# Kernel tuning notes

Measured on AMD Instinct MI355X. Metric: run time of the kernel, lower is better.

Reference implementation:

```python
import jax, jax.numpy as jnp
import numpy as np

D_MODEL = 1024
D_STATE = 16
N_LAYERS = 2
EXPAND = 2
D_CONV = 4
D_INNER = EXPAND * D_MODEL
DT_RANK = D_MODEL // 16  # 64
B, L = 2, 1024


def setup_inputs() -> dict:
    key = jax.random.key(0)
    ks = jax.random.split(key, 8)
    rn = lambda k, shape, s: jax.random.normal(k, shape, jnp.float32) * s
    x = rn(ks[0], (B, L, D_MODEL), 1.0)
    in_proj_w = rn(ks[1], (N_LAYERS, 2 * D_INNER, D_MODEL), D_MODEL ** -0.5)
    conv_w = rn(ks[2], (N_LAYERS, D_INNER, 1, D_CONV), D_CONV ** -0.5)
    conv_b = jnp.zeros((N_LAYERS, D_INNER), jnp.float32)
    x_proj_w = rn(ks[3], (N_LAYERS, DT_RANK + 2 * D_STATE, D_INNER), D_INNER ** -0.5)
    dt_proj_w = rn(ks[4], (N_LAYERS, D_INNER, DT_RANK), DT_RANK ** -0.5)
    dt_proj_b = rn(ks[5], (N_LAYERS, D_INNER), 0.1)
    # canonical Mamba init: A = -exp(A_log), A_log = log(1..d_state)
    A_log = jnp.tile(jnp.log(jnp.arange(1, D_STATE + 1, dtype=jnp.float32)), (N_LAYERS, D_INNER, 1))
    Dp = jnp.ones((N_LAYERS, D_INNER), jnp.float32)
    out_proj_w = rn(ks[6], (N_LAYERS, D_MODEL, D_INNER), D_INNER ** -0.5)
    ln_g = jnp.ones((N_LAYERS, D_MODEL), jnp.float32)
    ln_b = jnp.zeros((N_LAYERS, D_MODEL), jnp.float32)
    fn_g = jnp.ones((D_MODEL,), jnp.float32)
    fn_b = jnp.zeros((D_MODEL,), jnp.float32)
    return dict(x=x, ln_g=ln_g, ln_b=ln_b, in_proj_w=in_proj_w, conv_w=conv_w,
                conv_b=conv_b, x_proj_w=x_proj_w, dt_proj_w=dt_proj_w,
                dt_proj_b=dt_proj_b, A_log=A_log, Dp=Dp, out_proj_w=out_proj_w,
                fn_g=fn_g, fn_b=fn_b)


def _ln(x, g, b):
    m = jnp.mean(x, -1, keepdims=True)
    v = jnp.mean((x - m) ** 2, -1, keepdims=True)
    return (x - m) * jax.lax.rsqrt(v + 1e-5) * g + b


def _mamba_block(x, in_w, cw, cb, xpw, dtw, dtb, A_log, Dp, ow):
    Bb = x.shape[0]
    # input projection -> [B, L, 2*d_inner]
    xz = jnp.einsum('bld,ed->ble', x, in_w)
    u, res = jnp.split(xz, 2, axis=-1)
    # causal depthwise conv over time (torch: padding=3 then [..., :L])
    uc = jax.lax.conv_general_dilated(
        u.transpose(0, 2, 1), cw, (1,), [(D_CONV - 1, 0)],
        dimension_numbers=('NCH', 'OIH', 'NCH'), feature_group_count=D_INNER)
    u = jax.nn.silu(uc.transpose(0, 2, 1) + cb)  # [B, L, d_inner]
    # input-dependent dt, B, C
    xdbl = jnp.einsum('ble,fe->blf', u, xpw)
    dt, Bc, Cc = jnp.split(xdbl, [DT_RANK, DT_RANK + D_STATE], axis=-1)
    delta = jax.nn.softplus(jnp.einsum('blr,dr->bld', dt, dtw) + dtb)  # [B,L,d_inner]
    A = -jnp.exp(A_log)  # [d_inner, d_state]

    def step(h, inp):
        d_t, B_t, C_t, u_t = inp  # [B,d_inner],[B,d_state],[B,d_state],[B,d_inner]
        h = jnp.exp(d_t[:, :, None] * A) * h + (d_t * u_t)[:, :, None] * B_t[:, None, :]
        y = jnp.einsum('bds,bs->bd', h, C_t)
        return h, y

    xs = (delta.transpose(1, 0, 2), Bc.transpose(1, 0, 2),
          Cc.transpose(1, 0, 2), u.transpose(1, 0, 2))
    h0 = jnp.zeros((Bb, D_INNER, D_STATE), x.dtype)
    _, ys = jax.lax.scan(step, h0, xs)
    y = ys.transpose(1, 0, 2) + u * Dp
    y = y * jax.nn.silu(res)
    return jnp.einsum('ble,de->bld', y, ow)


def reference(x, ln_g, ln_b, in_proj_w, conv_w, conv_b, x_proj_w, dt_proj_w,
              dt_proj_b, A_log, Dp, out_proj_w, fn_g, fn_b):
    for i in range(N_LAYERS):
        x = x + _mamba_block(_ln(x, ln_g[i], ln_b[i]), in_proj_w[i], conv_w[i],
                             conv_b[i], x_proj_w[i], dt_proj_w[i], dt_proj_b[i],
                             A_log[i], Dp[i], out_proj_w[i])
    # dropout is identity in eval mode
    return _ln(x, fn_g, fn_b)
```

## Files before the change

kernel.cpp:

```cpp
#include <hip/hip_runtime.h>
#include <hip/hip_bf16.h>
#include <math.h>
#include <stdint.h>

#define DMODEL 1024
#define DSTATE 16
#define DINNER 2048
#define DTRANK 64
#define NB 2
#define LSEQ 1024
#define ROWS (NB*LSEQ)
#define NCH 64
#define LCH (LSEQ/NCH)
#define KSPLIT 8

typedef __bf16 bf16_t;
typedef __bf16 bf16x8 __attribute__((ext_vector_type(8)));
typedef __bf16 bf16x4 __attribute__((ext_vector_type(4)));
typedef float  f32x4  __attribute__((ext_vector_type(4)));

#define AS1(p) ((const __attribute__((address_space(1))) void*)(p))
#define AS3(p) ((__attribute__((address_space(3))) void*)(uint32_t)(uintptr_t)(p))

static __device__ __forceinline__ float sigmoidf_(float x){ return 1.f/(1.f+__expf(-x)); }
static __device__ __forceinline__ float softplusf_(float x){ return fmaxf(x,0.f) + log1pf(__expf(-fabsf(x))); }

__global__ __launch_bounds__(256) void cvt_kernel(const float* __restrict__ in,
    bf16_t* __restrict__ out, int n4)
{
  int i = blockIdx.x*256 + threadIdx.x;
  if (i < n4){
    float4 v = ((const float4*)in)[i];
    bf16x4 o = { (bf16_t)v.x, (bf16_t)v.y, (bf16_t)v.z, (bf16_t)v.w };
    ((bf16x4*)out)[i] = o;
  }
}

template<int OUTBF>
__global__ __launch_bounds__(256) void ln_kernel(const float* __restrict__ x,
    const float* __restrict__ g, const float* __restrict__ b,
    float* __restrict__ outf, bf16_t* __restrict__ outb)
{
  int row = blockIdx.x;
  float4 v = ((const float4*)(x + (size_t)row*DMODEL))[threadIdx.x];
  float s  = v.x+v.y+v.z+v.w;
  float s2 = v.x*v.x+v.y*v.y+v.z*v.z+v.w*v.w;
  #pragma unroll
  for (int off=32; off>=1; off>>=1){ s += __shfl_xor(s,off); s2 += __shfl_xor(s2,off); }
  __shared__ float red[8];
  int lane = threadIdx.x & 63, wid = threadIdx.x >> 6;
  if (lane==0){ red[wid]=s; red[4+wid]=s2; }
  __syncthreads();
  float ts  = red[0]+red[1]+red[2]+red[3];
  float ts2 = red[4]+red[5]+red[6]+red[7];
  float mean = ts*(1.f/DMODEL);
  float var  = ts2*(1.f/DMODEL) - mean*mean;
  float rstd = rsqrtf(var + 1e-5f);
  float4 gv = ((const float4*)g)[threadIdx.x];
  float4 bv = ((const float4*)b)[threadIdx.x];
  float4 o;
  o.x=(v.x-mean)*rstd*gv.x+bv.x;
  o.y=(v.y-mean)*rstd*gv.y+bv.y;
  o.z=(v.z-mean)*rstd*gv.z+bv.z;
  o.w=(v.w-mean)*rstd*gv.w+bv.w;
  if (OUTBF){
    bf16x4 ob = { (bf16_t)o.x, (bf16_t)o.y, (bf16_t)o.z, (bf16_t)o.w };
    ((bf16x4*)(outb + (size_t)row*DMODEL))[threadIdx.x] = ob;
  } else {
    ((float4*)(outf + (size_t)row*DMODEL))[threadIdx.x] = o;
  }
}

#define GBM 128
#define GBN 128
#define GBK 64

template<int EPI, bool NGUARD, bool SWZ>
__global__ __launch_bounds__(256) void gemm_bf16(
    const bf16_t* __restrict__ A, int lda,
    const bf16_t* __restrict__ W, int ldw,
    float* __restrict__ C, int ldc,
    int M, int N, int K,
    const float* __restrict__ bias,
    const float* __restrict__ addsrc,
    bf16_t* __restrict__ C2)
{
  __shared__ __align__(16) char lds[65536];
  const int tid  = threadIdx.x;
  const int lane = tid & 63, wid = tid >> 6;
  const int wr = wid >> 1, wc = wid & 1;
  const int frow = lane & 15, kgrp = lane >> 4;

  int bx = blockIdx.x, by = blockIdx.y;
  if (SWZ) {
    int gx = gridDim.x, gy = gridDim.y;
    int bid = by*gx + bx;
    int q = (gx*gy) >> 3;
    int nid = (bid & 7)*q + (bid >> 3);
    int stripH = gy << 3;
    int strip = nid / stripH;
    int rem   = nid % stripH;
    bx = (strip << 3) + (rem & 7);
    by = rem >> 3;
  }
  const int m0 = by*GBM, n0 = bx*GBN;
  const int srow  = (lane >> 3);
  const int scolb = (lane & 7) * 16;

  f32x4 acc[4][4];
  #pragma unroll
  for (int i=0;i<4;i++)
    #pragma unroll
    for (int j=0;j<4;j++)
      acc[i][j] = (f32x4){0.f,0.f,0.f,0.f};

  auto STAGE = [&](int k0, char* sAb, char* sBb){
    #pragma unroll
    for (int r=0;r<4;++r){
      int ci  = r*4 + wid;
      int row = ci*8 + srow;
      {
        const char* src = (const char*)A + ((size_t)(m0+row)*lda + k0)*2 + scolb;
        __builtin_amdgcn_global_load_lds(AS1(src), AS3(sAb + ci*1024), 16, 0, 0);
      }
      {
        int grow = n0 + row;
        if (NGUARD) grow = (grow < N) ? grow : (N-1);
        const char* src = (const char*)W + ((size_t)grow*ldw + k0)*2 + scolb;
        __builtin_amdgcn_global_load_lds(AS1(src), AS3(sBb + ci*1024), 16, 0, 0);
      }
    }
  };

  const int ksl = K / gridDim.z;
  const int kb  = blockIdx.z * ksl;
  const int nt  = ksl / GBK;

  STAGE(kb, lds, lds + 16384);
  __syncthreads();
  int cur = 0;
  for (int t = 0; t < nt; ++t) {
    char* cA = lds + cur*32768;
    char* cB = cA + 16384;
    if (t+1 < nt) {
      char* nA = lds + (cur^1)*32768;
      STAGE(kb + (t+1)*GBK, nA, nA + 16384);
    }
    #pragma unroll
    for (int ks=0; ks<2; ++ks){
      bf16x8 af[4], bfr[4];
      #pragma unroll
      for (int i=0;i<4;i++)
        af[i] = *(const bf16x8*)(cA + (wr*64 + i*16 + frow)*128 + ks*64 + kgrp*16);
      #pragma unroll
      for (int j=0;j<4;j++)
        bfr[j] = *(const bf16x8*)(cB + (wc*64 + j*16 + frow)*128 + ks*64 + kgrp*16);
      #pragma unroll
      for (int i=0;i<4;i++)
        #pragma unroll
        for (int j=0;j<4;j++)
          acc[i][j] = __builtin_amdgcn_mfma_f32_16x16x32_bf16(af[i], bfr[j], acc[i][j], 0, 0, 0);
    }
    __syncthreads();
    cur ^= 1;
  }

  if (EPI==4) {
    #pragma unroll
    for (int i=0;i<4;i++){
      int rbase = wr*64 + i*16 + kgrp*4;
      #pragma unroll
      for (int j=0;j<4;j++){
        int col = wc*64 + j*16 + frow;
        #pragma unroll
        for (int q=0;q<4;q++){
          int row = rbase + q;
          int byte = (row<<8) + (col<<1);
          byte ^= (row & 7) << 4;
          *(bf16_t*)(lds + byte) = (bf16_t)acc[i][j][q];
        }
      }
    }
    __syncthreads();
    int r = tid >> 1;
    int hb = (tid & 1) << 7;
    size_t gbase = (size_t)(m0 + r)*ldc + n0 + ((tid & 1) << 6);
    #pragma unroll
    for (int i=0;i<8;i++){
      int byte = (r<<8) + hb + (i<<4);
      byte ^= (r & 7) << 4;
      bf16x8 v = *(const bf16x8*)(lds + byte);
      *(bf16x8*)(C2 + gbase + (i<<3)) = v;
    }
    return;
  }

  float* Cw = (EPI==5) ? (C + (size_t)blockIdx.z*(size_t)M*ldc) : C;
  #pragma unroll
  for (int i=0;i<4;i++){
    int rbase = m0 + wr*64 + i*16 + kgrp*4;
    #pragma unroll
    for (int j=0;j<4;j++){
      int col = n0 + wc*64 + j*16 + frow;
      if (NGUARD && col >= N) continue;
      #pragma unroll
      for (int q=0;q<4;q++){
        float v = acc[i][j][q];
        int row = rbase + q;
        if (EPI==1) v = softplusf_(v + bias[col]);
        if (EPI==2) v += addsrc[(size_t)row*ldc + col];
        Cw[(size_t)row*ldc + col] = v;
      }
    }
  }
}

__global__ __launch_bounds__(256) void xp_reduce(
    const float* __restrict__ part, float* __restrict__ xdbl, bf16_t* __restrict__ xdbl_b)
{
  int idx = blockIdx.x*256 + threadIdx.x;
  float s = 0.f;
  #pragma unroll
  for (int k=0;k<KSPLIT;k++) s += part[(size_t)k*ROWS*96 + idx];
  xdbl[idx] = s;
  xdbl_b[idx] = (bf16_t)s;
}

__global__ __launch_bounds__(256) void conv_silu_kernel(
    const bf16_t* __restrict__ xzb, const float* __restrict__ cw,
    const float* __restrict__ cb, bf16_t* __restrict__ ub)
{
  int idx = blockIdx.x*256 + threadIdx.x;
  int d  = idx & (DINNER-1);
  int bl = idx >> 11;
  int l  = bl & (LSEQ-1);
  const bf16_t* col = xzb + (size_t)bl*(2*DINNER) + d;
  float w0=cw[d*4+0], w1=cw[d*4+1], w2=cw[d*4+2], w3=cw[d*4+3];
  float x3 = (float)col[0];
  float x2 = (l>=1) ? (float)col[-(ptrdiff_t)(2*DINNER)]  : 0.f;
  float x1 = (l>=2) ? (float)col[-(ptrdiff_t)(4*DINNER)]  : 0.f;
  float x0 = (l>=3) ? (float)col[-(ptrdiff_t)(6*DINNER)]  : 0.f;
  float acc = cb[d] + w0*x0 + w1*x1 + w2*x2 + w3*x3;
  float uu = acc * sigmoidf_(acc);
  ub[(size_t)bl*DINNER + d] = (bf16_t)uu;
}


__global__ __launch_bounds__(256) void scan_phase1(
    const float* __restrict__ delta, const bf16_t* __restrict__ u,
    const float* __restrict__ xdbl, const float* __restrict__ A_log,
    float* __restrict__ hout, float* __restrict__ sumd)
{
  __shared__ __align__(16) float bcs[LCH][32];
  int tid = threadIdx.x;
  int gid = blockIdx.x*256 + tid;
  int d = gid & (DINNER-1);
  int c = (gid >> 11) & (NCH-1);
  int b = gid >> 17;
  int l0 = c*LCH;
  #pragma unroll
  for (int i=0;i<2;i++){
    int ii = tid + i*256;
    int r = ii >> 5, q = ii & 31;
    bcs[r][q] = xdbl[(size_t)(b*LSEQ + l0 + r)*96 + DTRANK + q];
  }
  __syncthreads();

  f32x4 A4[4];
  #pragma unroll
  for (int si=0;si<4;si++){
    float4 al = ((const float4*)(A_log + d*DSTATE))[si];
    A4[si] = (f32x4){-__expf(al.x), -__expf(al.y), -__expf(al.z), -__expf(al.w)};
  }
  const float*  drow = delta + ((size_t)(b*LSEQ + l0))*DINNER + d;
  const bf16_t* urow = u     + ((size_t)(b*LSEQ + l0))*DINNER + d;
  f32x4 h[4] = {};
  float sd = 0.f;
  for (int l=0; l<LCH; ++l) {
    float dv = drow[(size_t)l*DINNER];
    float uv = (float)urow[(size_t)l*DINNER];
    float du = dv*uv;
    sd += dv;
    const f32x4* bl = (const f32x4*)&bcs[l][0];
    #pragma unroll
    for (int si=0;si<4;si++){
      f32x4 e;
      e[0]=__expf(dv*A4[si][0]); e[1]=__expf(dv*A4[si][1]);
      e[2]=__expf(dv*A4[si][2]); e[3]=__expf(dv*A4[si][3]);
      h[si] = e*h[si] + du*bl[si];
    }
  }
  float* hp = hout + (((size_t)(b*NCH + c))*DINNER + d)*DSTATE;
  #pragma unroll
  for (int si=0;si<4;si++) ((f32x4*)hp)[si] = h[si];
  sumd[((size_t)(b*NCH + c))*DINNER + d] = sd;
}

__global__ __launch_bounds__(256) void scan_phase2(
    float* __restrict__ hout, const float* __restrict__ sumd,
    const float* __restrict__ A_log)
{
  int gid = blockIdx.x*256 + threadIdx.x;
  int s = gid & (DSTATE-1);
  int d = (gid >> 4) & (DINNER-1);
  int b = gid >> 15;
  float A = -__expf(A_log[d*DSTATE+s]);
  float h = 0.f;
  for (int c=0; c<NCH; ++c) {
    size_t hi = (((size_t)(b*NCH + c))*DINNER + d)*DSTATE + s;
    float tmp = hout[hi];
    hout[hi] = h;
    float P = __expf(A * sumd[((size_t)(b*NCH + c))*DINNER + d]);
    h = P*h + tmp;
  }
}

__global__ __launch_bounds__(256) void scan_phase3(
    const float* __restrict__ delta, bf16_t* ysb,
    const bf16_t* u,
    const bf16_t* __restrict__ xzb,
    const float* __restrict__ xdbl,
    const float* __restrict__ A_log,
    const float* __restrict__ Dp,
    const float* __restrict__ hin)
{
  __shared__ __align__(16) float bcs[LCH][32];
  int tid = threadIdx.x;
  int gid = blockIdx.x*256 + tid;
  int d = gid & (DINNER-1);
  int c = (gid >> 11) & (NCH-1);
  int b = gid >> 17;
  int l0 = c*LCH;
  #pragma unroll
  for (int i=0;i<2;i++){
    int ii = tid + i*256;
    int r = ii >> 5, q = ii & 31;
    bcs[r][q] = xdbl[(size_t)(b*LSEQ + l0 + r)*96 + DTRANK + q];
  }
  __syncthreads();

  f32x4 A4[4];
  #pragma unroll
  for (int si=0;si<4;si++){
    float4 al = ((const float4*)(A_log + d*DSTATE))[si];
    A4[si] = (f32x4){-__expf(al.x), -__expf(al.y), -__expf(al.z), -__expf(al.w)};
  }
  float Dpd = Dp[d];
  f32x4 h[4];
  const float* hp = hin + (((size_t)(b*NCH + c))*DINNER + d)*DSTATE;
  #pragma unroll
  for (int si=0;si<4;si++) h[si] = ((const f32x4*)hp)[si];

  const float*  drow = delta + ((size_t)(b*LSEQ + l0))*DINNER + d;
  const bf16_t* urow = u     + ((size_t)(b*LSEQ + l0))*DINNER + d;
  const bf16_t* rrow = xzb   + ((size_t)(b*LSEQ + l0))*2*DINNER + DINNER + d;
  bf16_t* yrow = ysb + ((size_t)(b*LSEQ + l0))*DINNER + d;
  for (int l=0; l<LCH; ++l) {
    float dv = drow[(size_t)l*DINNER];
    float uv = (float)urow[(size_t)l*DINNER];
    float rv = (float)rrow[(size_t)l*2*DINNER];
    float du = dv*uv;
    const f32x4* bl = (const f32x4*)&bcs[l][0];
    f32x4 yv = {};
    #pragma unroll
    for (int si=0;si<4;si++){
      f32x4 e;
      e[0]=__expf(dv*A4[si][0]); e[1]=__expf(dv*A4[si][1]);
      e[2]=__expf(dv*A4[si][2]); e[3]=__expf(dv*A4[si][3]);
      h[si] = e*h[si] + du*bl[si];
      yv += h[si]*bl[4+si];
    }
    float y = yv[0]+yv[1]+yv[2]+yv[3];
    y = (y + uv*Dpd) * (rv * sigmoidf_(rv));
    yrow[(size_t)l*DINNER] = (bf16_t)y;
  }
}

extern "C" void kernel_launch(void* const* d_in, const int* in_sizes, int n_in,
                              void* d_out, int out_size, void* d_ws, size_t ws_size,
                              hipStream_t stream)
{
  const float* x      = (const float*)d_in[0];
  const float* ln_g   = (const float*)d_in[1];
  const float* ln_b   = (const float*)d_in[2];
  const float* in_w   = (const float*)d_in[3];
  const float* conv_w = (const float*)d_in[4];
  const float* conv_b = (const float*)d_in[5];
  const float* xp_w   = (const float*)d_in[6];
  const float* dt_w   = (const float*)d_in[7];
  const float* dt_b   = (const float*)d_in[8];
  const float* A_log  = (const float*)d_in[9];
  const float* Dp     = (const float*)d_in[10];
  const float* out_w  = (const float*)d_in[11];
  const float* fn_g   = (const float*)d_in[12];
  const float* fn_b   = (const float*)d_in[13];
  float* out = (float*)d_out;

  char* p = (char*)d_ws;
  auto alloc = [&](size_t bytes)->char*{ char* r = p; p += (bytes + 255) & ~(size_t)255; return r; };

  const size_t N_INW = (size_t)2*2*DINNER*DMODEL;
  const size_t N_XPW = (size_t)2*96*DINNER;
  const size_t N_DTW = (size_t)2*DINNER*DTRANK;
  const size_t N_OUTW= (size_t)2*DMODEL*DINNER;

  bf16_t* inw_b  = (bf16_t*)alloc(N_INW*2);
  bf16_t* xpw_b  = (bf16_t*)alloc(N_XPW*2);
  bf16_t* dtw_b  = (bf16_t*)alloc(N_DTW*2);
  bf16_t* outw_b = (bf16_t*)alloc(N_OUTW*2);
  float*  x_cur  = (float*) alloc((size_t)ROWS*DMODEL*4);
  bf16_t* xn_b   = (bf16_t*)alloc((size_t)ROWS*DMODEL*2);
  bf16_t* xzb    = (bf16_t*)alloc((size_t)ROWS*2*DINNER*2);
  bf16_t* ub_b   = (bf16_t*)alloc((size_t)ROWS*DINNER*2);
  float*  xdbl   = (float*) alloc((size_t)ROWS*96*4);
  bf16_t* xdbl_b = (bf16_t*)alloc((size_t)ROWS*96*2);
  float*  xpart  = (float*) alloc((size_t)KSPLIT*ROWS*96*4);
  float*  delta  = (float*) alloc((size_t)ROWS*DINNER*4);
  float*  hout   = (float*) alloc((size_t)NB*NCH*DINNER*DSTATE*4);
  float*  sumd   = (float*) alloc((size_t)NB*NCH*DINNER*4);
  bf16_t* ys_b   = ub_b;

  cvt_kernel<<<(int)((N_INW/4 +255)/256),256,0,stream>>>(in_w,  inw_b,  (int)(N_INW/4));
  cvt_kernel<<<(int)((N_XPW/4 +255)/256),256,0,stream>>>(xp_w,  xpw_b,  (int)(N_XPW/4));
  cvt_kernel<<<(int)((N_DTW/4 +255)/256),256,0,stream>>>(dt_w,  dtw_b,  (int)(N_DTW/4));
  cvt_kernel<<<(int)((N_OUTW/4+255)/256),256,0,stream>>>(out_w, outw_b, (int)(N_OUTW/4));

  for (int layer=0; layer<2; ++layer) {
    const float* xin = (layer==0) ? x : x_cur;
    const float* Al  = A_log + (size_t)layer*DINNER*DSTATE;
    ln_kernel<1><<<ROWS,256,0,stream>>>(xin, ln_g+layer*DMODEL, ln_b+layer*DMODEL, nullptr, xn_b);
    gemm_bf16<4,false,true><<<dim3(2*DINNER/GBN, ROWS/GBM),256,0,stream>>>(
        xn_b, DMODEL, inw_b + (size_t)layer*2*DINNER*DMODEL, DMODEL,
        nullptr, 2*DINNER, ROWS, 2*DINNER, DMODEL, nullptr, nullptr, xzb);
    conv_silu_kernel<<<(ROWS*DINNER)/256,256,0,stream>>>(
        xzb, conv_w + (size_t)layer*DINNER*4, conv_b + (size_t)layer*DINNER, ub_b);
    gemm_bf16<5,true,false><<<dim3(1, ROWS/GBM, KSPLIT),256,0,stream>>>(
        ub_b, DINNER, xpw_b + (size_t)layer*96*DINNER, DINNER,
        xpart, 96, ROWS, 96, DINNER, nullptr, nullptr, nullptr);
    xp_reduce<<<(ROWS*96)/256,256,0,stream>>>(xpart, xdbl, xdbl_b);
    gemm_bf16<1,false,true><<<dim3(DINNER/GBN, ROWS/GBM),256,0,stream>>>(
        xdbl_b, 96, dtw_b + (size_t)layer*DINNER*DTRANK, DTRANK,
        delta, DINNER, ROWS, DINNER, DTRANK,
        dt_b + (size_t)layer*DINNER, nullptr, nullptr);
    scan_phase1<<<(NB*NCH*DINNER)/256,256,0,stream>>>(delta, ub_b, xdbl, Al, hout, sumd);
    scan_phase2<<<(NB*DINNER*DSTATE)/256,256,0,stream>>>(hout, sumd, Al);
    scan_phase3<<<(NB*NCH*DINNER)/256,256,0,stream>>>(
        delta, ys_b, ub_b, xzb, xdbl, Al, Dp + (size_t)layer*DINNER, hout);
    gemm_bf16<2,false,true><<<dim3(DMODEL/GBN, ROWS/GBM),256,0,stream>>>(
        ys_b, DINNER, outw_b + (size_t)layer*DMODEL*DINNER, DINNER,
        x_cur, DMODEL, ROWS, DMODEL, DINNER, nullptr, xin, nullptr);
  }
  ln_kernel<0><<<ROWS,256,0,stream>>>(x_cur, fn_g, fn_b, out, nullptr);
}
```

Baseline: 445.5 us.

## Fuse dt projection into scan phases, merge weight casts, retile out_proj GEMM

```diff
diff --git a/kernel.cpp b/kernel.cpp
--- a/kernel.cpp
+++ b/kernel.cpp
@@ -12,7 +12,7 @@
 #define ROWS (NB*LSEQ)
 #define NCH 64
 #define LCH (LSEQ/NCH)
-#define KSPLIT 8
+#define KSPLIT 16
 
 typedef __bf16 bf16_t;
 typedef __bf16 bf16x8 __attribute__((ext_vector_type(8)));
@@ -25,15 +25,30 @@
 static __device__ __forceinline__ float sigmoidf_(float x){ return 1.f/(1.f+__expf(-x)); }
 static __device__ __forceinline__ float softplusf_(float x){ return fmaxf(x,0.f) + log1pf(__expf(-fabsf(x))); }
 
-__global__ __launch_bounds__(256) void cvt_kernel(const float* __restrict__ in,
-    bf16_t* __restrict__ out, int n4)
-{
-  int i = blockIdx.x*256 + threadIdx.x;
-  if (i < n4){
-    float4 v = ((const float4*)in)[i];
-    bf16x4 o = { (bf16_t)v.x, (bf16_t)v.y, (bf16_t)v.z, (bf16_t)v.w };
-    ((bf16x4*)out)[i] = o;
-  }
+#define N_INW  ((size_t)2*2*DINNER*DMODEL)
+#define N_XPW  ((size_t)2*96*DINNER)
+#define N_DTW  ((size_t)2*DINNER*DTRANK)
+#define N_OUTW ((size_t)2*DMODEL*DINNER)
+
+__global__ __launch_bounds__(256) void cvt_all(
+    const float* __restrict__ inw, const float* __restrict__ xpw,
+    const float* __restrict__ dtw, const float* __restrict__ outw,
+    bf16_t* __restrict__ o_inw, bf16_t* __restrict__ o_xpw,
+    bf16_t* __restrict__ o_dtw, bf16_t* __restrict__ o_outw)
+{
+  const int n_in = (int)(N_INW/4), n_xp = (int)(N_XPW/4),
+            n_dt = (int)(N_DTW/4), n_out = (int)(N_OUTW/4);
+  int j = blockIdx.x*256 + threadIdx.x;
+  const float* src; bf16_t* dst;
+  if (j < n_in) { src = inw; dst = o_inw; }
+  else { j -= n_in;
+    if (j < n_xp) { src = xpw; dst = o_xpw; }
+    else { j -= n_xp;
+      if (j < n_dt) { src = dtw; dst = o_dtw; }
+      else { j -= n_dt; if (j >= n_out) return; src = outw; dst = o_outw; } } }
+  float4 v = ((const float4*)src)[j];
+  bf16x4 o = { (bf16_t)v.x, (bf16_t)v.y, (bf16_t)v.z, (bf16_t)v.w };
+  ((bf16x4*)dst)[j] = o;
 }
 
 template<int OUTBF>
@@ -72,10 +87,9 @@
 }
 
 #define GBM 128
-#define GBN 128
 #define GBK 64
 
-template<int EPI, bool NGUARD, bool SWZ>
+template<int EPI, bool NGUARD, bool SWZ, int JR>
 __global__ __launch_bounds__(256) void gemm_bf16(
     const bf16_t* __restrict__ A, int lda,
     const bf16_t* __restrict__ W, int ldw,
@@ -85,7 +99,10 @@
     const float* __restrict__ addsrc,
     bf16_t* __restrict__ C2)
 {
-  __shared__ __align__(16) char lds[65536];
+  constexpr int GBN  = JR*32;
+  constexpr int SBB  = GBN*128;
+  constexpr int BUFB = 16384 + SBB;
+  __shared__ __align__(16) char lds[2*BUFB];
   const int tid  = threadIdx.x;
   const int lane = tid & 63, wid = tid >> 6;
   const int wr = wid >> 1, wc = wid & 1;
@@ -107,11 +124,11 @@
   const int srow  = (lane >> 3);
   const int scolb = (lane & 7) * 16;
 
-  f32x4 acc[4][4];
+  f32x4 acc[4][JR];
   #pragma unroll
   for (int i=0;i<4;i++)
     #pragma unroll
-    for (int j=0;j<4;j++)
+    for (int j=0;j<JR;j++)
       acc[i][j] = (f32x4){0.f,0.f,0.f,0.f};
 
   auto STAGE = [&](int k0, char* sAb, char* sBb){
@@ -119,16 +136,17 @@
     for (int r=0;r<4;++r){
       int ci  = r*4 + wid;
       int row = ci*8 + srow;
-      {
-        const char* src = (const char*)A + ((size_t)(m0+row)*lda + k0)*2 + scolb;
-        __builtin_amdgcn_global_load_lds(AS1(src), AS3(sAb + ci*1024), 16, 0, 0);
-      }
-      {
-        int grow = n0 + row;
-        if (NGUARD) grow = (grow < N) ? grow : (N-1);
-        const char* src = (const char*)W + ((size_t)grow*ldw + k0)*2 + scolb;
-        __builtin_amdgcn_global_load_lds(AS1(src), AS3(sBb + ci*1024), 16, 0, 0);
-      }
+      const char* src = (const char*)A + ((size_t)(m0+row)*lda + k0)*2 + scolb;
+      __builtin_amdgcn_global_load_lds(AS1(src), AS3(sAb + ci*1024), 16, 0, 0);
+    }
+    #pragma unroll
+    for (int r=0;r<JR;++r){
+      int ci  = r*4 + wid;
+      int row = ci*8 + srow;
+      int grow = n0 + row;
+      if (NGUARD) grow = (grow < N) ? grow : (N-1);
+      const char* src = (const char*)W + ((size_t)grow*ldw + k0)*2 + scolb;
+      __builtin_amdgcn_global_load_lds(AS1(src), AS3(sBb + ci*1024), 16, 0, 0);
     }
   };
 
@@ -140,32 +158,32 @@
   __syncthreads();
   int cur = 0;
   for (int t = 0; t < nt; ++t) {
-    char* cA = lds + cur*32768;
+    char* cA = lds + cur*BUFB;
     char* cB = cA + 16384;
     if (t+1 < nt) {
-      char* nA = lds + (cur^1)*32768;
+      char* nA = lds + (cur^1)*BUFB;
       STAGE(kb + (t+1)*GBK, nA, nA + 16384);
     }
     #pragma unroll
     for (int ks=0; ks<2; ++ks){
-      bf16x8 af[4], bfr[4];
+      bf16x8 af[4], bfr[JR];
       #pragma unroll
       for (int i=0;i<4;i++)
         af[i] = *(const bf16x8*)(cA + (wr*64 + i*16 + frow)*128 + ks*64 + kgrp*16);
       #pragma unroll
-      for (int j=0;j<4;j++)
-        bfr[j] = *(const bf16x8*)(cB + (wc*64 + j*16 + frow)*128 + ks*64 + kgrp*16);
+      for (int j=0;j<JR;j++)
+        bfr[j] = *(const bf16x8*)(cB + (wc*(16*JR) + j*16 + frow)*128 + ks*64 + kgrp*16);
       #pragma unroll
       for (int i=0;i<4;i++)
         #pragma unroll
-        for (int j=0;j<4;j++)
+        for (int j=0;j<JR;j++)
           acc[i][j] = __builtin_amdgcn_mfma_f32_16x16x32_bf16(af[i], bfr[j], acc[i][j], 0, 0, 0);
     }
     __syncthreads();
     cur ^= 1;
   }
 
-  if (EPI==4) {
+  if constexpr (EPI==4 && JR==4) {
     #pragma unroll
     for (int i=0;i<4;i++){
       int rbase = wr*64 + i*16 + kgrp*4;
@@ -200,8 +218,8 @@
   for (int i=0;i<4;i++){
     int rbase = m0 + wr*64 + i*16 + kgrp*4;
     #pragma unroll
-    for (int j=0;j<4;j++){
-      int col = n0 + wc*64 + j*16 + frow;
+    for (int j=0;j<JR;j++){
+      int col = n0 + wc*(16*JR) + j*16 + frow;
       if (NGUARD && col >= N) continue;
       #pragma unroll
       for (int q=0;q<4;q++){
@@ -216,14 +234,13 @@
 }
 
 __global__ __launch_bounds__(256) void xp_reduce(
-    const float* __restrict__ part, float* __restrict__ xdbl, bf16_t* __restrict__ xdbl_b)
+    const float* __restrict__ part, float* __restrict__ xdbl)
 {
   int idx = blockIdx.x*256 + threadIdx.x;
   float s = 0.f;
   #pragma unroll
   for (int k=0;k<KSPLIT;k++) s += part[(size_t)k*ROWS*96 + idx];
   xdbl[idx] = s;
-  xdbl_b[idx] = (bf16_t)s;
 }
 
 __global__ __launch_bounds__(256) void conv_silu_kernel(
@@ -247,11 +264,13 @@
 
 
 __global__ __launch_bounds__(256) void scan_phase1(
-    const float* __restrict__ delta, const bf16_t* __restrict__ u,
-    const float* __restrict__ xdbl, const float* __restrict__ A_log,
+    const bf16_t* __restrict__ u,
+    const float* __restrict__ xdbl, const bf16_t* __restrict__ dtw,
+    const float* __restrict__ dtb,  const float* __restrict__ A_log,
     float* __restrict__ hout, float* __restrict__ sumd)
 {
   __shared__ __align__(16) float bcs[LCH][32];
+  __shared__ __align__(16) float dts[LCH][DTRANK];
   int tid = threadIdx.x;
   int gid = blockIdx.x*256 + tid;
   int d = gid & (DINNER-1);
@@ -264,7 +283,34 @@
     int r = ii >> 5, q = ii & 31;
     bcs[r][q] = xdbl[(size_t)(b*LSEQ + l0 + r)*96 + DTRANK + q];
   }
+  #pragma unroll
+  for (int i=0;i<4;i++){
+    int ii = tid + i*256;
+    int r = ii >> 6, q = ii & 63;
+    dts[r][q] = xdbl[(size_t)(b*LSEQ + l0 + r)*96 + q];
+  }
   __syncthreads();
+
+  float dly[LCH];
+  {
+    float w[DTRANK];
+    const bf16x8* wp = (const bf16x8*)(dtw + (size_t)d*DTRANK);
+    #pragma unroll
+    for (int k8=0;k8<8;k8++){
+      bf16x8 wv = wp[k8];
+      #pragma unroll
+      for (int e=0;e<8;e++) w[k8*8+e] = (float)wv[e];
+    }
+    float bias = dtb[d];
+    #pragma unroll
+    for (int l=0;l<LCH;l++){
+      f32x4 a4 = {};
+      const f32x4* dl = (const f32x4*)&dts[l][0];
+      #pragma unroll
+      for (int k4=0;k4<16;k4++) a4 += dl[k4] * (*(const f32x4*)&w[k4*4]);
+      dly[l] = softplusf_((a4[0]+a4[1]+a4[2]+a4[3]) + bias);
+    }
+  }
 
   f32x4 A4[4];
   #pragma unroll
@@ -272,12 +318,12 @@
     float4 al = ((const float4*)(A_log + d*DSTATE))[si];
     A4[si] = (f32x4){-__expf(al.x), -__expf(al.y), -__expf(al.z), -__expf(al.w)};
   }
-  const float*  drow = delta + ((size_t)(b*LSEQ + l0))*DINNER + d;
-  const bf16_t* urow = u     + ((size_t)(b*LSEQ + l0))*DINNER + d;
+  const bf16_t* urow = u + ((size_t)(b*LSEQ + l0))*DINNER + d;
   f32x4 h[4] = {};
   float sd = 0.f;
+  #pragma unroll
   for (int l=0; l<LCH; ++l) {
-    float dv = drow[(size_t)l*DINNER];
+    float dv = dly[l];
     float uv = (float)urow[(size_t)l*DINNER];
     float du = dv*uv;
     sd += dv;
@@ -316,15 +362,17 @@
 }
 
 __global__ __launch_bounds__(256) void scan_phase3(
-    const float* __restrict__ delta, bf16_t* ysb,
-    const bf16_t* u,
+    bf16_t* ysb, const bf16_t* u,
     const bf16_t* __restrict__ xzb,
     const float* __restrict__ xdbl,
+    const bf16_t* __restrict__ dtw,
+    const float* __restrict__ dtb,
     const float* __restrict__ A_log,
     const float* __restrict__ Dp,
     const float* __restrict__ hin)
 {
   __shared__ __align__(16) float bcs[LCH][32];
+  __shared__ __align__(16) float dts[LCH][DTRANK];
   int tid = threadIdx.x;
   int gid = blockIdx.x*256 + tid;
   int d = gid & (DINNER-1);
@@ -337,7 +385,34 @@
     int r = ii >> 5, q = ii & 31;
     bcs[r][q] = xdbl[(size_t)(b*LSEQ + l0 + r)*96 + DTRANK + q];
   }
+  #pragma unroll
+  for (int i=0;i<4;i++){
+    int ii = tid + i*256;
+    int r = ii >> 6, q = ii & 63;
+    dts[r][q] = xdbl[(size_t)(b*LSEQ + l0 + r)*96 + q];
+  }
   __syncthreads();
+
+  float dly[LCH];
+  {
+    float w[DTRANK];
+    const bf16x8* wp = (const bf16x8*)(dtw + (size_t)d*DTRANK);
+    #pragma unroll
+    for (int k8=0;k8<8;k8++){
+      bf16x8 wv = wp[k8];
+      #pragma unroll
+      for (int e=0;e<8;e++) w[k8*8+e] = (float)wv[e];
+    }
+    float bias = dtb[d];
+    #pragma unroll
+    for (int l=0;l<LCH;l++){
+      f32x4 a4 = {};
+      const f32x4* dl = (const f32x4*)&dts[l][0];
+      #pragma unroll
+      for (int k4=0;k4<16;k4++) a4 += dl[k4] * (*(const f32x4*)&w[k4*4]);
+      dly[l] = softplusf_((a4[0]+a4[1]+a4[2]+a4[3]) + bias);
+    }
+  }
 
   f32x4 A4[4];
   #pragma unroll
@@ -351,12 +426,12 @@
   #pragma unroll
   for (int si=0;si<4;si++) h[si] = ((const f32x4*)hp)[si];
 
-  const float*  drow = delta + ((size_t)(b*LSEQ + l0))*DINNER + d;
-  const bf16_t* urow = u     + ((size_t)(b*LSEQ + l0))*DINNER + d;
-  const bf16_t* rrow = xzb   + ((size_t)(b*LSEQ + l0))*2*DINNER + DINNER + d;
+  const bf16_t* urow = u   + ((size_t)(b*LSEQ + l0))*DINNER + d;
+  const bf16_t* rrow = xzb + ((size_t)(b*LSEQ + l0))*2*DINNER + DINNER + d;
   bf16_t* yrow = ysb + ((size_t)(b*LSEQ + l0))*DINNER + d;
+  #pragma unroll
   for (int l=0; l<LCH; ++l) {
-    float dv = drow[(size_t)l*DINNER];
+    float dv = dly[l];
     float uv = (float)urow[(size_t)l*DINNER];
     float rv = (float)rrow[(size_t)l*2*DINNER];
     float du = dv*uv;
@@ -399,11 +474,6 @@
   char* p = (char*)d_ws;
   auto alloc = [&](size_t bytes)->char*{ char* r = p; p += (bytes + 255) & ~(size_t)255; return r; };
 
-  const size_t N_INW = (size_t)2*2*DINNER*DMODEL;
-  const size_t N_XPW = (size_t)2*96*DINNER;
-  const size_t N_DTW = (size_t)2*DINNER*DTRANK;
-  const size_t N_OUTW= (size_t)2*DMODEL*DINNER;
-
   bf16_t* inw_b  = (bf16_t*)alloc(N_INW*2);
   bf16_t* xpw_b  = (bf16_t*)alloc(N_XPW*2);
   bf16_t* dtw_b  = (bf16_t*)alloc(N_DTW*2);
@@ -413,40 +483,38 @@
   bf16_t* xzb    = (bf16_t*)alloc((size_t)ROWS*2*DINNER*2);
   bf16_t* ub_b   = (bf16_t*)alloc((size_t)ROWS*DINNER*2);
   float*  xdbl   = (float*) alloc((size_t)ROWS*96*4);
-  bf16_t* xdbl_b = (bf16_t*)alloc((size_t)ROWS*96*2);
   float*  xpart  = (float*) alloc((size_t)KSPLIT*ROWS*96*4);
-  float*  delta  = (float*) alloc((size_t)ROWS*DINNER*4);
   float*  hout   = (float*) alloc((size_t)NB*NCH*DINNER*DSTATE*4);
   float*  sumd   = (float*) alloc((size_t)NB*NCH*DINNER*4);
   bf16_t* ys_b   = ub_b;
 
-  cvt_kernel<<<(int)((N_INW/4 +255)/256),256,0,stream>>>(in_w,  inw_b,  (int)(N_INW/4));
-  cvt_kernel<<<(int)((N_XPW/4 +255)/256),256,0,stream>>>(xp_w,  xpw_b,  (int)(N_XPW/4));
-  cvt_kernel<<<(int)((N_DTW/4 +255)/256),256,0,stream>>>(dt_w,  dtw_b,  (int)(N_DTW/4));
-  cvt_kernel<<<(int)((N_OUTW/4+255)/256),256,0,stream>>>(out_w, outw_b, (int)(N_OUTW/4));
+  {
+    size_t total4 = (N_INW + N_XPW + N_DTW + N_OUTW)/4;
+    cvt_all<<<(int)((total4+255)/256),256,0,stream>>>(
+        in_w, xp_w, dt_w, out_w, inw_b, xpw_b, dtw_b, outw_b);
+  }
 
   for (int layer=0; layer<2; ++layer) {
     const float* xin = (layer==0) ? x : x_cur;
     const float* Al  = A_log + (size_t)layer*DINNER*DSTATE;
+    const bf16_t* dtwb = dtw_b + (size_t)layer*DINNER*DTRANK;
+    const float*  dtbb = dt_b  + (size_t)layer*DINNER;
     ln_kernel<1><<<ROWS,256,0,stream>>>(xin, ln_g+layer*DMODEL, ln_b+layer*DMODEL, nullptr, xn_b);
-    gemm_bf16<4,false,true><<<dim3(2*DINNER/GBN, ROWS/GBM),256,0,stream>>>(
+    gemm_bf16<4,false,true,4><<<dim3(2*DINNER/128, ROWS/GBM),256,0,stream>>>(
         xn_b, DMODEL, inw_b + (size_t)layer*2*DINNER*DMODEL, DMODEL,
         nullptr, 2*DINNER, ROWS, 2*DINNER, DMODEL, nullptr, nullptr, xzb);
     conv_silu_kernel<<<(ROWS*DINNER)/256,256,0,stream>>>(
         xzb, conv_w + (size_t)layer*DINNER*4, conv_b + (size_t)layer*DINNER, ub_b);
-    gemm_bf16<5,true,false><<<dim3(1, ROWS/GBM, KSPLIT),256,0,stream>>>(
+    gemm_bf16<5,true,false,4><<<dim3(1, ROWS/GBM, KSPLIT),256,0,stream>>>(
         ub_b, DINNER, xpw_b + (size_t)layer*96*DINNER, DINNER,
         xpart, 96, ROWS, 96, DINNER, nullptr, nullptr, nullptr);
-    xp_reduce<<<(ROWS*96)/256,256,0,stream>>>(xpart, xdbl, xdbl_b);
-    gemm_bf16<1,false,true><<<dim3(DINNER/GBN, ROWS/GBM),256,0,stream>>>(
-        xdbl_b, 96, dtw_b + (size_t)layer*DINNER*DTRANK, DTRANK,
-        delta, DINNER, ROWS, DINNER, DTRANK,
-        dt_b + (size_t)layer*DINNER, nullptr, nullptr);
-    scan_phase1<<<(NB*NCH*DINNER)/256,256,0,stream>>>(delta, ub_b, xdbl, Al, hout, sumd);
+    xp_reduce<<<(ROWS*96)/256,256,0,stream>>>(xpart, xdbl);
+    scan_phase1<<<(NB*NCH*DINNER)/256,256,0,stream>>>(
+        ub_b, xdbl, dtwb, dtbb, Al, hout, sumd);
     scan_phase2<<<(NB*DINNER*DSTATE)/256,256,0,stream>>>(hout, sumd, Al);
     scan_phase3<<<(NB*NCH*DINNER)/256,256,0,stream>>>(
-        delta, ys_b, ub_b, xzb, xdbl, Al, Dp + (size_t)layer*DINNER, hout);
-    gemm_bf16<2,false,true><<<dim3(DMODEL/GBN, ROWS/GBM),256,0,stream>>>(
+        ys_b, ub_b, xzb, xdbl, dtwb, dtbb, Al, Dp + (size_t)layer*DINNER, hout);
+    gemm_bf16<2,false,true,2><<<dim3(DMODEL/64, ROWS/GBM),256,0,stream>>>(
         ys_b, DINNER, outw_b + (size_t)layer*DMODEL*DINNER, DINNER,
         x_cur, DMODEL, ROWS, DMODEL, DINNER, nullptr, xin, nullptr);
   }
```

Result: slower. 467.3 us (+4.9%).

## Retune scan chunks, split-K, out-proj tile width, exp2 scan, fused weight cast

Applied to the files above, without the earlier changes.

```diff
diff --git a/kernel.cpp b/kernel.cpp
--- a/kernel.cpp
+++ b/kernel.cpp
@@ -10,9 +10,9 @@
 #define NB 2
 #define LSEQ 1024
 #define ROWS (NB*LSEQ)
-#define NCH 64
+#define NCH 128
 #define LCH (LSEQ/NCH)
-#define KSPLIT 8
+#define KSPLIT 16
 
 typedef __bf16 bf16_t;
 typedef __bf16 bf16x8 __attribute__((ext_vector_type(8)));
@@ -24,16 +24,32 @@
 
 static __device__ __forceinline__ float sigmoidf_(float x){ return 1.f/(1.f+__expf(-x)); }
 static __device__ __forceinline__ float softplusf_(float x){ return fmaxf(x,0.f) + log1pf(__expf(-fabsf(x))); }
-
-__global__ __launch_bounds__(256) void cvt_kernel(const float* __restrict__ in,
-    bf16_t* __restrict__ out, int n4)
-{
-  int i = blockIdx.x*256 + threadIdx.x;
-  if (i < n4){
-    float4 v = ((const float4*)in)[i];
-    bf16x4 o = { (bf16_t)v.x, (bf16_t)v.y, (bf16_t)v.z, (bf16_t)v.w };
-    ((bf16x4*)out)[i] = o;
-  }
+#define LOG2E 1.44269504f
+
+#define N_INW  ((size_t)2*2*DINNER*DMODEL)
+#define N_XPW  ((size_t)2*96*DINNER)
+#define N_DTW  ((size_t)2*DINNER*DTRANK)
+#define N_OUTW ((size_t)2*DMODEL*DINNER)
+
+__global__ __launch_bounds__(256) void cvt_all(
+    const float* __restrict__ inw, const float* __restrict__ xpw,
+    const float* __restrict__ dtw, const float* __restrict__ outw,
+    bf16_t* __restrict__ o_inw, bf16_t* __restrict__ o_xpw,
+    bf16_t* __restrict__ o_dtw, bf16_t* __restrict__ o_outw)
+{
+  const int n_in = (int)(N_INW/4), n_xp = (int)(N_XPW/4),
+            n_dt = (int)(N_DTW/4), n_out = (int)(N_OUTW/4);
+  int j = blockIdx.x*256 + threadIdx.x;
+  const float* src; bf16_t* dst;
+  if (j < n_in) { src = inw; dst = o_inw; }
+  else { j -= n_in;
+    if (j < n_xp) { src = xpw; dst = o_xpw; }
+    else { j -= n_xp;
+      if (j < n_dt) { src = dtw; dst = o_dtw; }
+      else { j -= n_dt; if (j >= n_out) return; src = outw; dst = o_outw; } } }
+  float4 v = ((const float4*)src)[j];
+  bf16x4 o = { (bf16_t)v.x, (bf16_t)v.y, (bf16_t)v.z, (bf16_t)v.w };
+  ((bf16x4*)dst)[j] = o;
 }
 
 template<int OUTBF>
@@ -72,10 +88,9 @@
 }
 
 #define GBM 128
-#define GBN 128
 #define GBK 64
 
-template<int EPI, bool NGUARD, bool SWZ>
+template<int EPI, bool NGUARD, bool SWZ, int JR>
 __global__ __launch_bounds__(256) void gemm_bf16(
     const bf16_t* __restrict__ A, int lda,
     const bf16_t* __restrict__ W, int ldw,
@@ -85,7 +100,10 @@
     const float* __restrict__ addsrc,
     bf16_t* __restrict__ C2)
 {
-  __shared__ __align__(16) char lds[65536];
+  constexpr int GBN  = JR*32;
+  constexpr int SBB  = GBN*128;
+  constexpr int BUFB = 16384 + SBB;
+  __shared__ __align__(16) char lds[2*BUFB];
   const int tid  = threadIdx.x;
   const int lane = tid & 63, wid = tid >> 6;
   const int wr = wid >> 1, wc = wid & 1;
@@ -107,11 +125,11 @@
   const int srow  = (lane >> 3);
   const int scolb = (lane & 7) * 16;
 
-  f32x4 acc[4][4];
+  f32x4 acc[4][JR];
   #pragma unroll
   for (int i=0;i<4;i++)
     #pragma unroll
-    for (int j=0;j<4;j++)
+    for (int j=0;j<JR;j++)
       acc[i][j] = (f32x4){0.f,0.f,0.f,0.f};
 
   auto STAGE = [&](int k0, char* sAb, char* sBb){
@@ -119,16 +137,17 @@
     for (int r=0;r<4;++r){
       int ci  = r*4 + wid;
       int row = ci*8 + srow;
-      {
-        const char* src = (const char*)A + ((size_t)(m0+row)*lda + k0)*2 + scolb;
-        __builtin_amdgcn_global_load_lds(AS1(src), AS3(sAb + ci*1024), 16, 0, 0);
-      }
-      {
-        int grow = n0 + row;
-        if (NGUARD) grow = (grow < N) ? grow : (N-1);
-        const char* src = (const char*)W + ((size_t)grow*ldw + k0)*2 + scolb;
-        __builtin_amdgcn_global_load_lds(AS1(src), AS3(sBb + ci*1024), 16, 0, 0);
-      }
+      const char* src = (const char*)A + ((size_t)(m0+row)*lda + k0)*2 + scolb;
+      __builtin_amdgcn_global_load_lds(AS1(src), AS3(sAb + ci*1024), 16, 0, 0);
+    }
+    #pragma unroll
+    for (int r=0;r<JR;++r){
+      int ci  = r*4 + wid;
+      int row = ci*8 + srow;
+      int grow = n0 + row;
+      if (NGUARD) grow = (grow < N) ? grow : (N-1);
+      const char* src = (const char*)W + ((size_t)grow*ldw + k0)*2 + scolb;
+      __builtin_amdgcn_global_load_lds(AS1(src), AS3(sBb + ci*1024), 16, 0, 0);
     }
   };
 
@@ -140,32 +159,32 @@
   __syncthreads();
   int cur = 0;
   for (int t = 0; t < nt; ++t) {
-    char* cA = lds + cur*32768;
+    char* cA = lds + cur*BUFB;
     char* cB = cA + 16384;
     if (t+1 < nt) {
-      char* nA = lds + (cur^1)*32768;
+      char* nA = lds + (cur^1)*BUFB;
       STAGE(kb + (t+1)*GBK, nA, nA + 16384);
     }
     #pragma unroll
     for (int ks=0; ks<2; ++ks){
-      bf16x8 af[4], bfr[4];
+      bf16x8 af[4], bfr[JR];
       #pragma unroll
       for (int i=0;i<4;i++)
         af[i] = *(const bf16x8*)(cA + (wr*64 + i*16 + frow)*128 + ks*64 + kgrp*16);
       #pragma unroll
-      for (int j=0;j<4;j++)
-        bfr[j] = *(const bf16x8*)(cB + (wc*64 + j*16 + frow)*128 + ks*64 + kgrp*16);
+      for (int j=0;j<JR;j++)
+        bfr[j] = *(const bf16x8*)(cB + (wc*(16*JR) + j*16 + frow)*128 + ks*64 + kgrp*16);
       #pragma unroll
       for (int i=0;i<4;i++)
         #pragma unroll
-        for (int j=0;j<4;j++)
+        for (int j=0;j<JR;j++)
           acc[i][j] = __builtin_amdgcn_mfma_f32_16x16x32_bf16(af[i], bfr[j], acc[i][j], 0, 0, 0);
     }
     __syncthreads();
     cur ^= 1;
   }
 
-  if (EPI==4) {
+  if constexpr (EPI==4 && JR==4) {
     #pragma unroll
     for (int i=0;i<4;i++){
       int rbase = wr*64 + i*16 + kgrp*4;
@@ -200,8 +219,8 @@
   for (int i=0;i<4;i++){
     int rbase = m0 + wr*64 + i*16 + kgrp*4;
     #pragma unroll
-    for (int j=0;j<4;j++){
-      int col = n0 + wc*64 + j*16 + frow;
+    for (int j=0;j<JR;j++){
+      int col = n0 + wc*(16*JR) + j*16 + frow;
       if (NGUARD && col >= N) continue;
       #pragma unroll
       for (int q=0;q<4;q++){
@@ -256,12 +275,10 @@
   int gid = blockIdx.x*256 + tid;
   int d = gid & (DINNER-1);
   int c = (gid >> 11) & (NCH-1);
-  int b = gid >> 17;
+  int b = gid >> 18;
   int l0 = c*LCH;
-  #pragma unroll
-  for (int i=0;i<2;i++){
-    int ii = tid + i*256;
-    int r = ii >> 5, q = ii & 31;
+  {
+    int r = tid >> 5, q = tid & 31;
     bcs[r][q] = xdbl[(size_t)(b*LSEQ + l0 + r)*96 + DTRANK + q];
   }
   __syncthreads();
@@ -270,12 +287,14 @@
   #pragma unroll
   for (int si=0;si<4;si++){
     float4 al = ((const float4*)(A_log + d*DSTATE))[si];
-    A4[si] = (f32x4){-__expf(al.x), -__expf(al.y), -__expf(al.z), -__expf(al.w)};
+    A4[si] = (f32x4){-LOG2E*__expf(al.x), -LOG2E*__expf(al.y),
+                     -LOG2E*__expf(al.z), -LOG2E*__expf(al.w)};
   }
   const float*  drow = delta + ((size_t)(b*LSEQ + l0))*DINNER + d;
   const bf16_t* urow = u     + ((size_t)(b*LSEQ + l0))*DINNER + d;
   f32x4 h[4] = {};
   float sd = 0.f;
+  #pragma unroll
   for (int l=0; l<LCH; ++l) {
     float dv = drow[(size_t)l*DINNER];
     float uv = (float)urow[(size_t)l*DINNER];
@@ -285,8 +304,8 @@
     #pragma unroll
     for (int si=0;si<4;si++){
       f32x4 e;
-      e[0]=__expf(dv*A4[si][0]); e[1]=__expf(dv*A4[si][1]);
-      e[2]=__expf(dv*A4[si][2]); e[3]=__expf(dv*A4[si][3]);
+      e[0]=exp2f(dv*A4[si][0]); e[1]=exp2f(dv*A4[si][1]);
+      e[2]=exp2f(dv*A4[si][2]); e[3]=exp2f(dv*A4[si][3]);
       h[si] = e*h[si] + du*bl[si];
     }
   }
@@ -304,13 +323,13 @@
   int s = gid & (DSTATE-1);
   int d = (gid >> 4) & (DINNER-1);
   int b = gid >> 15;
-  float A = -__expf(A_log[d*DSTATE+s]);
+  float A = -LOG2E*__expf(A_log[d*DSTATE+s]);
   float h = 0.f;
   for (int c=0; c<NCH; ++c) {
     size_t hi = (((size_t)(b*NCH + c))*DINNER + d)*DSTATE + s;
     float tmp = hout[hi];
     hout[hi] = h;
-    float P = __expf(A * sumd[((size_t)(b*NCH + c))*DINNER + d]);
+    float P = exp2f(A * sumd[((size_t)(b*NCH + c))*DINNER + d]);
     h = P*h + tmp;
   }
 }
@@ -329,12 +348,10 @@
   int gid = blockIdx.x*256 + tid;
   int d = gid & (DINNER-1);
   int c = (gid >> 11) & (NCH-1);
-  int b = gid >> 17;
+  int b = gid >> 18;
   int l0 = c*LCH;
-  #pragma unroll
-  for (int i=0;i<2;i++){
-    int ii = tid + i*256;
-    int r = ii >> 5, q = ii & 31;
+  {
+    int r = tid >> 5, q = tid & 31;
     bcs[r][q] = xdbl[(size_t)(b*LSEQ + l0 + r)*96 + DTRANK + q];
   }
   __syncthreads();
@@ -343,7 +360,8 @@
   #pragma unroll
   for (int si=0;si<4;si++){
     float4 al = ((const float4*)(A_log + d*DSTATE))[si];
-    A4[si] = (f32x4){-__expf(al.x), -__expf(al.y), -__expf(al.z), -__expf(al.w)};
+    A4[si] = (f32x4){-LOG2E*__expf(al.x), -LOG2E*__expf(al.y),
+                     -LOG2E*__expf(al.z), -LOG2E*__expf(al.w)};
   }
   float Dpd = Dp[d];
   f32x4 h[4];
@@ -355,6 +373,7 @@
   const bf16_t* urow = u     + ((size_t)(b*LSEQ + l0))*DINNER + d;
   const bf16_t* rrow = xzb   + ((size_t)(b*LSEQ + l0))*2*DINNER + DINNER + d;
   bf16_t* yrow = ysb + ((size_t)(b*LSEQ + l0))*DINNER + d;
+  #pragma unroll
   for (int l=0; l<LCH; ++l) {
     float dv = drow[(size_t)l*DINNER];
     float uv = (float)urow[(size_t)l*DINNER];
@@ -365,8 +384,8 @@
     #pragma unroll
     for (int si=0;si<4;si++){
       f32x4 e;
-      e[0]=__expf(dv*A4[si][0]); e[1]=__expf(dv*A4[si][1]);
-      e[2]=__expf(dv*A4[si][2]); e[3]=__expf(dv*A4[si][3]);
+      e[0]=exp2f(dv*A4[si][0]); e[1]=exp2f(dv*A4[si][1]);
+      e[2]=exp2f(dv*A4[si][2]); e[3]=exp2f(dv*A4[si][3]);
       h[si] = e*h[si] + du*bl[si];
       yv += h[si]*bl[4+si];
     }
@@ -399,11 +418,6 @@
   char* p = (char*)d_ws;
   auto alloc = [&](size_t bytes)->char*{ char* r = p; p += (bytes + 255) & ~(size_t)255; return r; };
 
-  const size_t N_INW = (size_t)2*2*DINNER*DMODEL;
-  const size_t N_XPW = (size_t)2*96*DINNER;
-  const size_t N_DTW = (size_t)2*DINNER*DTRANK;
-  const size_t N_OUTW= (size_t)2*DMODEL*DINNER;
-
   bf16_t* inw_b  = (bf16_t*)alloc(N_INW*2);
   bf16_t* xpw_b  = (bf16_t*)alloc(N_XPW*2);
   bf16_t* dtw_b  = (bf16_t*)alloc(N_DTW*2);
@@ -420,25 +434,26 @@
   float*  sumd   = (float*) alloc((size_t)NB*NCH*DINNER*4);
   bf16_t* ys_b   = ub_b;
 
-  cvt_kernel<<<(int)((N_INW/4 +255)/256),256,0,stream>>>(in_w,  inw_b,  (int)(N_INW/4));
-  cvt_kernel<<<(int)((N_XPW/4 +255)/256),256,0,stream>>>(xp_w,  xpw_b,  (int)(N_XPW/4));
-  cvt_kernel<<<(int)((N_DTW/4 +255)/256),256,0,stream>>>(dt_w,  dtw_b,  (int)(N_DTW/4));
-  cvt_kernel<<<(int)((N_OUTW/4+255)/256),256,0,stream>>>(out_w, outw_b, (int)(N_OUTW/4));
+  {
+    size_t total4 = (N_INW + N_XPW + N_DTW + N_OUTW)/4;
+    cvt_all<<<(int)((total4+255)/256),256,0,stream>>>(
+        in_w, xp_w, dt_w, out_w, inw_b, xpw_b, dtw_b, outw_b);
+  }
 
   for (int layer=0; layer<2; ++layer) {
     const float* xin = (layer==0) ? x : x_cur;
     const float* Al  = A_log + (size_t)layer*DINNER*DSTATE;
     ln_kernel<1><<<ROWS,256,0,stream>>>(xin, ln_g+layer*DMODEL, ln_b+layer*DMODEL, nullptr, xn_b);
-    gemm_bf16<4,false,true><<<dim3(2*DINNER/GBN, ROWS/GBM),256,0,stream>>>(
+    gemm_bf16<4,false,true,4><<<dim3(2*DINNER/128, ROWS/GBM),256,0,stream>>>(
         xn_b, DMODEL, inw_b + (size_t)layer*2*DINNER*DMODEL, DMODEL,
         nullptr, 2*DINNER, ROWS, 2*DINNER, DMODEL, nullptr, nullptr, xzb);
     conv_silu_kernel<<<(ROWS*DINNER)/256,256,0,stream>>>(
         xzb, conv_w + (size_t)layer*DINNER*4, conv_b + (size_t)layer*DINNER, ub_b);
-    gemm_bf16<5,true,false><<<dim3(1, ROWS/GBM, KSPLIT),256,0,stream>>>(
+    gemm_bf16<5,true,false,4><<<dim3(1, ROWS/GBM, KSPLIT),256,0,stream>>>(
         ub_b, DINNER, xpw_b + (size_t)layer*96*DINNER, DINNER,
         xpart, 96, ROWS, 96, DINNER, nullptr, nullptr, nullptr);
     xp_reduce<<<(ROWS*96)/256,256,0,stream>>>(xpart, xdbl, xdbl_b);
-    gemm_bf16<1,false,true><<<dim3(DINNER/GBN, ROWS/GBM),256,0,stream>>>(
+    gemm_bf16<1,false,true,4><<<dim3(DINNER/128, ROWS/GBM),256,0,stream>>>(
         xdbl_b, 96, dtw_b + (size_t)layer*DINNER*DTRANK, DTRANK,
         delta, DINNER, ROWS, DINNER, DTRANK,
         dt_b + (size_t)layer*DINNER, nullptr, nullptr);
@@ -446,7 +461,7 @@
     scan_phase2<<<(NB*DINNER*DSTATE)/256,256,0,stream>>>(hout, sumd, Al);
     scan_phase3<<<(NB*NCH*DINNER)/256,256,0,stream>>>(
         delta, ys_b, ub_b, xzb, xdbl, Al, Dp + (size_t)layer*DINNER, hout);
-    gemm_bf16<2,false,true><<<dim3(DMODEL/GBN, ROWS/GBM),256,0,stream>>>(
+    gemm_bf16<2,false,true,2><<<dim3(DMODEL/64, ROWS/GBM),256,0,stream>>>(
         ys_b, DINNER, outw_b + (size_t)layer*DMODEL*DINNER, DINNER,
         x_cur, DMODEL, ROWS, DMODEL, DINNER, nullptr, xin, nullptr);
   }
```

After: 457.2 us. +2.6%, slower.
